# Optimization experiments

Measured on AMD Instinct MI355X. Metric: run time of the kernel, lower is better.

The kernel has to match this reference:

```python
import jax, jax.numpy as jnp
import numpy as np

TEXT_DIM = 1024
FEAT_DIM = 1024
NUM_HEADS = 16
HEAD_DIM = FEAT_DIM // NUM_HEADS
EPS = 1e-6


def rms_norm(x, w):
    # LlamaRMSNorm: compute in fp32, scale by learned weight
    xf = x.astype(jnp.float32)
    var = jnp.mean(xf * xf, axis=-1, keepdims=True)
    return (xf * jax.lax.rsqrt(var + EPS)).astype(x.dtype) * w


def setup_inputs() -> dict:
    key = jax.random.key(0)
    ks = jax.random.split(key, 8)
    def xavier(k, shape, gain=1.0):
        fan_in, fan_out = shape[1], shape[0]
        lim = gain * np.sqrt(6.0 / (fan_in + fan_out))
        return jax.random.uniform(k, shape, jnp.float32, -lim, lim)
    return {
        "text": jax.random.normal(ks[0], (8, 512, TEXT_DIM), jnp.float32),
        "features": jax.random.normal(ks[1], (8, 1024, FEAT_DIM), jnp.float32),
        "W_q": xavier(ks[2], (FEAT_DIM, TEXT_DIM)),
        "b_q": jnp.zeros((FEAT_DIM,), jnp.float32),
        "W_k": xavier(ks[3], (FEAT_DIM, FEAT_DIM)),
        "b_k": jnp.zeros((FEAT_DIM,), jnp.float32),
        "W_o": xavier(ks[4], (FEAT_DIM, FEAT_DIM), gain=0.1),
        "b_o": jnp.zeros((FEAT_DIM,), jnp.float32),
        "g_feat": jnp.ones((FEAT_DIM,), jnp.float32),
        "g_q": jnp.ones((FEAT_DIM,), jnp.float32),
        "g_k": jnp.ones((FEAT_DIM,), jnp.float32),
    }


def reference(text, features, W_q, b_q, W_k, b_k, W_o, b_o, g_feat, g_q, g_k):
    B, T, _ = text.shape
    _, N, _ = features.shape
    feats = rms_norm(features, g_feat)                      # [B,N,Df]
    Q = rms_norm(text @ W_q.T + b_q, g_q)                   # [B,T,Df]
    K = rms_norm(feats @ W_k.T + b_k, g_k)                  # [B,N,Df]
    Qh = Q.reshape(B, T, NUM_HEADS, HEAD_DIM)
    Kh = K.reshape(B, N, NUM_HEADS, HEAD_DIM)
    Vh = feats.reshape(B, N, NUM_HEADS, HEAD_DIM)
    scores = jnp.einsum("bthd,bnhd->bhtn", Qh, Kh) / np.sqrt(HEAD_DIM).astype(np.float32)
    attn = jax.nn.softmax(scores, axis=-1)                  # [B,H,T,N]
    out = jnp.einsum("bhtn,bnhd->bthd", attn, Vh).reshape(B, T, FEAT_DIM)
    return out @ W_o.T + b_o
```

## Files before the change

### kernel.cpp

```cpp
#include <hip/hip_runtime.h>
#include <hip/hip_bf16.h>


typedef unsigned short u16;
typedef __bf16 bf16x8 __attribute__((ext_vector_type(8)));
typedef float f32x4 __attribute__((ext_vector_type(4)));

extern "C" __device__ float __ocml_native_exp2_f32(float);

__device__ inline f32x4 mfma16(bf16x8 a, bf16x8 b, f32x4 c) {
    return __builtin_amdgcn_mfma_f32_16x16x32_bf16(a, b, c, 0, 0, 0);
}

__device__ inline u16 f2bf(float f) {
    union { float f; unsigned u; } v; v.f = f;
    unsigned r = v.u + 0x7fffu + ((v.u >> 16) & 1u);
    return (u16)(r >> 16);
}

__device__ inline unsigned pk_bf16(float a, float b) {
    union { float f; unsigned u; } x, y; x.f = a; y.f = b;
    return __builtin_amdgcn_perm(y.u + 0x8000u, x.u + 0x8000u, 0x07060302u);
}

__device__ inline unsigned cvt_pk(float a, float b) {
    unsigned r;
    asm("v_cvt_pk_bf16_f32 %0, %1, %2" : "=v"(r) : "v"(a), "v"(b));
    return r;
}

__device__ inline void load_lds16(const void* g, void* l) {
    __builtin_amdgcn_global_load_lds(
        (const __attribute__((address_space(1))) void*)g,
        (__attribute__((address_space(3))) void*)l, 16, 0, 0);
}

__global__ __launch_bounds__(256) void cast_rows_kernel(const float* __restrict__ text,
                                                        const float* __restrict__ Wq,
                                                        const float* __restrict__ Wk,
                                                        const float* __restrict__ Wo,
                                                        const float* __restrict__ features,
                                                        const float* __restrict__ g_feat,
                                                        u16* __restrict__ otext, u16* __restrict__ oWq,
                                                        u16* __restrict__ oWk, u16* __restrict__ oWo,
                                                        u16* __restrict__ feats_bf,
                                                        float* __restrict__ qkss) {
    int blk = blockIdx.x, tid = threadIdx.x;
    if (blk < 7168) {
        int i = blk * 256 + tid;
        const float* src; u16* dst; int off;
        if (i < 1048576)      { src = text; dst = otext; off = i; }
        else if (i < 1310720) { src = Wq;   dst = oWq;   off = i - 1048576; }
        else if (i < 1572864) { src = Wk;   dst = oWk;   off = i - 1310720; }
        else                  { src = Wo;   dst = oWo;   off = i - 1572864; }
        float4 v = ((const float4*)src)[off];
        uint2 p; p.x = pk_bf16(v.x, v.y); p.y = pk_bf16(v.z, v.w);
        ((uint2*)dst)[off] = p;
    } else {
        int i2 = (blk - 7168) * 256 + tid;
        if (i2 < 12288) qkss[i2] = 0.0f;
        int row = (blk - 7168) * 4 + (tid >> 6);
        int lane = tid & 63;
        const float4* rp = (const float4*)(features + (size_t)row * 1024) + lane * 4;
        float4 v[4];
        float ss = 0.0f;
        #pragma unroll
        for (int i = 0; i < 4; ++i) {
            v[i] = rp[i];
            ss += v[i].x * v[i].x + v[i].y * v[i].y + v[i].z * v[i].z + v[i].w * v[i].w;
        }
        #pragma unroll
        for (int m = 1; m < 64; m <<= 1) ss += __shfl_xor(ss, m, 64);
        float rs = rsqrtf(ss * (1.0f / 1024.0f) + 1e-6f);
        const float4* gp = (const float4*)(g_feat) + lane * 4;
        union { unsigned u[8]; uint4 q[2]; } ob;
        #pragma unroll
        for (int i = 0; i < 4; ++i) {
            float4 gv = gp[i];
            ob.u[i * 2]     = pk_bf16(v[i].x * rs * gv.x, v[i].y * rs * gv.y);
            ob.u[i * 2 + 1] = pk_bf16(v[i].z * rs * gv.z, v[i].w * rs * gv.w);
        }
        uint4* dst = (uint4*)(feats_bf + (size_t)row * 1024 + lane * 16);
        dst[0] = ob.q[0];
        dst[1] = ob.q[1];
    }
}

__global__ __launch_bounds__(256) void normT_kernel(const u16* __restrict__ feats_bf,
                                                    u16* __restrict__ Vt) {
    __shared__ __align__(16) u16 tile[64][72];
    int tid = threadIdx.x, b = blockIdx.z;
    int n0 = blockIdx.x * 64, d0 = blockIdx.y * 64;
    int r = tid >> 2, cs = (tid & 3) * 16;
    int grow = b * 1024 + n0 + r;

    const uint4* src = (const uint4*)(feats_bf + (size_t)grow * 1024 + d0 + cs);
    union { u16 s[16]; uint4 v[2]; } ob;
    ob.v[0] = src[0];
    ob.v[1] = src[1];
    #pragma unroll
    for (int i = 0; i < 16; ++i) tile[r][cs + i] = ob.s[i];
    __syncthreads();
    union { u16 s[8]; uint4 v; } t0, t1;
    #pragma unroll
    for (int i = 0; i < 8; ++i) { t0.s[i] = tile[cs + i][r]; t1.s[i] = tile[cs + 8 + i][r]; }
    u16* tdst = Vt + ((size_t)(b * 1024 + d0 + r)) * 1024 + n0 + cs;
    *(uint4*)tdst = t0.v;
    *(uint4*)(tdst + 8) = t1.v;
}

template <bool BF16OUT, bool NORM>
__device__ __forceinline__ void gemm64_bk64(const u16* __restrict__ A, const u16* __restrict__ B,
                                            const float* __restrict__ bias,
                                            const float* __restrict__ gvec,
                                            float* __restrict__ ssout,
                                            void* __restrict__ Cout,
                                            int m_blk, int n_blk, int K, int N,
                                            u16* As, u16* Bs) {
    int tid = threadIdx.x, wave = tid >> 6, lane = tid & 63;
    int quad = lane >> 4, l15 = lane & 15;
    int wm = wave & 1, wn = wave >> 1;
    int srl = lane >> 3, scl = lane & 7;
    const int swz = (scl ^ srl) * 8;

    f32x4 acc[4][2] = {};

    auto stage = [&](int buf, int k0) {
        u16* Ad = As + buf * (128 * 64);
        u16* Bd = Bs + buf * (64 * 64);
        #pragma unroll
        for (int is = 0; is < 4; ++is) {
            int row = is * 32 + wave * 8 + srl;
            load_lds16(A + (size_t)(m_blk + row) * K + k0 + swz,
                       Ad + (is * 32 + wave * 8) * 64);
        }
        #pragma unroll
        for (int is = 0; is < 2; ++is) {
            int row = is * 32 + wave * 8 + srl;
            load_lds16(B + (size_t)(n_blk + row) * K + k0 + swz,
                       Bd + (is * 32 + wave * 8) * 64);
        }
    };

    stage(0, 0);
    __syncthreads();
    int cur = 0;

    for (int k0 = 0; k0 < K; k0 += 64) {
        if (k0 + 64 < K) stage(cur ^ 1, k0 + 64);

        const u16* Ar = As + cur * (128 * 64);
        const u16* Br = Bs + cur * (64 * 64);
        #pragma unroll
        for (int kh = 0; kh < 2; ++kh) {
            bf16x8 af[4], bfr[2];
            int co = ((kh * 4 + quad) ^ (l15 & 7)) * 8;
            #pragma unroll
            for (int t = 0; t < 4; ++t)
                af[t] = *(const bf16x8*)&Ar[(wm * 64 + t * 16 + l15) * 64 + co];
            #pragma unroll
            for (int t = 0; t < 2; ++t)
                bfr[t] = *(const bf16x8*)&Br[(wn * 32 + t * 16 + l15) * 64 + co];
            #pragma unroll
            for (int mt = 0; mt < 4; ++mt)
                #pragma unroll
                for (int nt = 0; nt < 2; ++nt)
                    acc[mt][nt] = mfma16(af[mt], bfr[nt], acc[mt][nt]);
        }
        __syncthreads();
        cur ^= 1;
    }

    float bv[2], gv[2];
    #pragma unroll
    for (int nt = 0; nt < 2; ++nt) {
        int col = n_blk + wn * 32 + nt * 16 + l15;
        bv[nt] = bias[col];
        if (NORM) gv[nt] = gvec[col];
    }
    #pragma unroll
    for (int mt = 0; mt < 4; ++mt) {
        int row0 = m_blk + wm * 64 + mt * 16 + quad * 4;
        #pragma unroll
        for (int nt = 0; nt < 2; ++nt)
            #pragma unroll
            for (int r = 0; r < 4; ++r)
                acc[mt][nt][r] += bv[nt];
        if (NORM) {
            f32x4 ss4 = {0.0f, 0.0f, 0.0f, 0.0f};
            #pragma unroll
            for (int nt = 0; nt < 2; ++nt)
                #pragma unroll
                for (int r = 0; r < 4; ++r)
                    ss4[r] += acc[mt][nt][r] * acc[mt][nt][r];
            #pragma unroll
            for (int m = 1; m < 16; m <<= 1)
                #pragma unroll
                for (int r = 0; r < 4; ++r)
                    ss4[r] += __shfl_xor(ss4[r], m, 64);
            if (l15 == 0) {
                #pragma unroll
                for (int r = 0; r < 4; ++r)
                    atomicAdd(&ssout[row0 + r], ss4[r]);
            }
        }
        #pragma unroll
        for (int nt = 0; nt < 2; ++nt) {
            int col = n_blk + wn * 32 + nt * 16 + l15;
            #pragma unroll
            for (int r = 0; r < 4; ++r) {
                float val = NORM ? acc[mt][nt][r] * gv[nt] : acc[mt][nt][r];
                if (BF16OUT) ((u16*)Cout)[(size_t)(row0 + r) * N + col] = f2bf(val);
                else       ((float*)Cout)[(size_t)(row0 + r) * N + col] = val;
            }
        }
    }
}

__global__ __launch_bounds__(256) void gemm_qk_kernel(const u16* __restrict__ text_bf,
                                                      const u16* __restrict__ Wq,
                                                      const u16* __restrict__ feats_bf,
                                                      const u16* __restrict__ Wk,
                                                      const float* __restrict__ b_q,
                                                      const float* __restrict__ b_k,
                                                      const float* __restrict__ g_q,
                                                      const float* __restrict__ g_k,
                                                      float* __restrict__ qkss,
                                                      u16* __restrict__ QK) {
    __shared__ __align__(16) u16 As[2 * 128 * 64];
    __shared__ __align__(16) u16 Bs[2 * 64 * 64];
    int id = blockIdx.x;
    if (id < 512) {
        gemm64_bk64<true, true>(text_bf, Wq, b_q, g_q, qkss, QK,
                                (id & 31) * 128, (id >> 5) * 64, 1024, 1024, As, Bs);
    } else {
        id -= 512;
        gemm64_bk64<true, true>(feats_bf, Wk, b_k, g_k, qkss + 4096, QK + 4096 * 1024,
                                (id & 63) * 128, (id >> 6) * 64, 1024, 1024, As, Bs);
    }
}

__global__ __launch_bounds__(256) void gemm_o_kernel(const u16* __restrict__ A,
                                                     const u16* __restrict__ B,
                                                     const float* __restrict__ bias,
                                                     float* __restrict__ C) {
    __shared__ __align__(16) u16 As[2 * 128 * 64];
    __shared__ __align__(16) u16 Bs[2 * 64 * 64];
    int id = blockIdx.x;
    gemm64_bk64<false, false>(A, B, bias, nullptr, nullptr, C,
                              (id & 31) * 128, (id >> 5) * 64, 1024, 1024, As, Bs);
}

__global__ __launch_bounds__(256, 4) void attn_kernel(const u16* __restrict__ Q,
                                                      const u16* __restrict__ K,
                                                      const u16* __restrict__ Vt,
                                                      const float* __restrict__ qkss,
                                                      u16* __restrict__ Out) {
    const float QSCALE = 0.18033688011112042f;
    int bh = blockIdx.x, qt = blockIdx.y;
    int b = bh >> 4, h = bh & 15;
    int tid = threadIdx.x, wave = tid >> 6, lane = tid & 63;
    int quad = lane >> 4, l15 = lane & 15;
    int wq = wave & 1, wn = wave >> 1;

    __shared__ __align__(16) u16 Ks[2][64 * 64];
    __shared__ __align__(16) u16 Vs[2][64 * 64];
    __shared__ __align__(16) u16 Plds[4][2 * 16 * 32];
    u16* Pw = &Plds[wave][0];
    const int pfs = (l15 >> 1) & 3;

    bf16x8 qf[2][2];
    float rsq[2];
    #pragma unroll
    for (int mt = 0; mt < 2; ++mt) {
        int qrow = b * 512 + qt * 64 + wq * 32 + mt * 16 + l15;
        const size_t qoff = (size_t)qrow * 1024 + h * 64 + quad * 8;
        qf[mt][0] = *(const bf16x8*)(Q + qoff);
        qf[mt][1] = *(const bf16x8*)(Q + qoff + 32);
        rsq[mt] = rsqrtf(qkss[qrow] * (1.0f / 1024.0f) + 1e-6f) * QSCALE;
    }
    const float* ssk = qkss + 4096 + b * 1024;

    int srl = lane >> 3, scl = lane & 7;
    const u16* Kbase = K + ((size_t)(b * 1024)) * 1024 + h * 64;
    const u16* Vbase = Vt + ((size_t)(b * 1024 + h * 64)) * 1024;

    __bf16 onev = (__bf16)1.0f;
    bf16x8 ones = {onev, onev, onev, onev, onev, onev, onev, onev};

    f32x4 o[2][4] = {};
    f32x4 lac[2] = {{0.0f, 0.0f, 0.0f, 0.0f}, {0.0f, 0.0f, 0.0f, 0.0f}};

    auto stage = [&](int buf, int n0) {
        #pragma unroll
        for (int j = 0; j < 2; ++j) {
            int row = wave * 16 + j * 8 + srl;
            load_lds16(Kbase + (size_t)(n0 + row) * 1024 + (scl ^ srl) * 8,
                       &Ks[buf][(wave * 16 + j * 8) * 64]);
            load_lds16(Vbase + (size_t)row * 1024 + n0 + (scl ^ srl) * 8,
                       &Vs[buf][(wave * 16 + j * 8) * 64]);
        }
    };

    stage(0, 0);
    __syncthreads();
    int cur = 0;

    for (int n0 = 0; n0 < 1024; n0 += 64) {
        if (n0 < 960) stage(cur ^ 1, n0 + 64);

        f32x4 s[2][2];
        __builtin_amdgcn_s_setprio(1);
        #pragma unroll
        for (int nt = 0; nt < 2; ++nt) {
            int R = wn * 32 + nt * 16 + l15;
            int c1 = (quad ^ (l15 & 7)) * 8;
            bf16x8 kf0 = *(const bf16x8*)&Ks[cur][R * 64 + c1];
            bf16x8 kf1 = *(const bf16x8*)&Ks[cur][R * 64 + (c1 ^ 32)];
            #pragma unroll
            for (int mt = 0; mt < 2; ++mt) {
                f32x4 z = {0.0f, 0.0f, 0.0f, 0.0f};
                s[mt][nt] = mfma16(kf0, qf[mt][0], z);
                s[mt][nt] = mfma16(kf1, qf[mt][1], s[mt][nt]);
            }
        }
        __builtin_amdgcn_s_setprio(0);

        #pragma unroll
        for (int nt = 0; nt < 2; ++nt) {
            int nb = n0 + wn * 32 + nt * 16 + quad * 4;
            f32x4 kss = *(const f32x4*)&ssk[nb];
            f32x4 rsn;
            #pragma unroll
            for (int r = 0; r < 4; ++r)
                rsn[r] = rsqrtf(kss[r] * (1.0f / 1024.0f) + 1e-6f);
            #pragma unroll
            for (int mt = 0; mt < 2; ++mt) {
                float e[4];
                #pragma unroll
                for (int r = 0; r < 4; ++r)
                    e[r] = __ocml_native_exp2_f32(fmaf(s[mt][nt][r], rsn[r] * rsq[mt], -16.0f));
                uint2 pk;
                pk.x = cvt_pk(e[0], e[1]);
                pk.y = cvt_pk(e[2], e[3]);
                *(uint2*)&Pw[mt * 512 + l15 * 32 + (((nt * 4 + quad) ^ (pfs << 1)) << 2)] = pk;
            }
        }

        bf16x8 pf[2], vf[4];
        #pragma unroll
        for (int mt = 0; mt < 2; ++mt)
            pf[mt] = *(const bf16x8*)&Pw[mt * 512 + l15 * 32 + ((quad ^ pfs) << 3)];
        #pragma unroll
        for (int dt = 0; dt < 4; ++dt) {
            int ch = ((wn * 4 + quad) ^ (l15 & 7)) * 8;
            vf[dt] = *(const bf16x8*)&Vs[cur][(dt * 16 + l15) * 64 + ch];
        }
        __builtin_amdgcn_s_setprio(1);
        #pragma unroll
        for (int mt = 0; mt < 2; ++mt) {
            lac[mt] = mfma16(ones, pf[mt], lac[mt]);
            #pragma unroll
            for (int dt = 0; dt < 4; ++dt)
                o[mt][dt] = mfma16(vf[dt], pf[mt], o[mt][dt]);
        }
        __builtin_amdgcn_s_setprio(0);

        __syncthreads();
        cur ^= 1;
    }

    float* Ored = (float*)&Ks[0][0];
    float* Lred = (float*)&Vs[0][0];
    if (wn == 1) {
        #pragma unroll
        for (int mt = 0; mt < 2; ++mt) {
            #pragma unroll
            for (int dt = 0; dt < 4; ++dt) {
                int c = mt * 4 + dt;
                *(f32x4*)&Ored[wq * 2048 + lane * 32 + ((c ^ (lane & 7)) << 2)] = o[mt][dt];
            }
            Lred[wq * 128 + lane * 2 + mt] = lac[mt][0];
        }
    }
    __syncthreads();
    if (wn == 0) {
        #pragma unroll
        for (int mt = 0; mt < 2; ++mt) {
            float il = 1.0f / (lac[mt][0] + Lred[wq * 128 + lane * 2 + mt]);
            size_t obase =
                ((size_t)(b * 512 + qt * 64 + wq * 32 + mt * 16 + l15)) * 1024 + h * 64 + quad * 4;
            #pragma unroll
            for (int dt = 0; dt < 4; ++dt) {
                int c = mt * 4 + dt;
                f32x4 oo = o[mt][dt] + *(const f32x4*)&Ored[wq * 2048 + lane * 32 + ((c ^ (lane & 7)) << 2)];
                uint2 pk;
                pk.x = cvt_pk(oo[0] * il, oo[1] * il);
                pk.y = cvt_pk(oo[2] * il, oo[3] * il);
                *(uint2*)(Out + obase + dt * 16) = pk;
            }
        }
    }
}

extern "C" void kernel_launch(void* const* d_in, const int* in_sizes, int n_in,
                              void* d_out, int out_size, void* d_ws, size_t ws_size,
                              hipStream_t stream) {
    const float* text     = (const float*)d_in[0];
    const float* features = (const float*)d_in[1];
    const float* W_q      = (const float*)d_in[2];
    const float* b_q      = (const float*)d_in[3];
    const float* W_k      = (const float*)d_in[4];
    const float* b_k      = (const float*)d_in[5];
    const float* W_o      = (const float*)d_in[6];
    const float* b_o      = (const float*)d_in[7];
    const float* g_feat   = (const float*)d_in[8];
    const float* g_q      = (const float*)d_in[9];
    const float* g_k      = (const float*)d_in[10];

    char* ws = (char*)d_ws;
    u16*   text_bf  = (u16*)(ws + 0);
    u16*   Wq_bf    = (u16*)(ws + 8388608);
    u16*   Wk_bf    = (u16*)(ws + 10485760);
    u16*   Wo_bf    = (u16*)(ws + 12582912);
    u16*   feats_bf = (u16*)(ws + 14680064);
    u16*   Vt       = (u16*)(ws + 31457280);
    u16*   QKbuf    = (u16*)(ws + 48234496);
    u16*   attn_bf  = (u16*)(ws + 73400320);
    float* qkss     = (float*)(ws + 81821696);

    cast_rows_kernel<<<9216, 256, 0, stream>>>(text, W_q, W_k, W_o, features, g_feat,
                                               text_bf, Wq_bf, Wk_bf, Wo_bf,
                                               feats_bf, qkss);
    normT_kernel<<<dim3(16, 16, 8), 256, 0, stream>>>(feats_bf, Vt);
    gemm_qk_kernel<<<1536, 256, 0, stream>>>(text_bf, Wq_bf, feats_bf, Wk_bf,
                                             b_q, b_k, g_q, g_k, qkss, QKbuf);
    attn_kernel<<<dim3(128, 8), 256, 0, stream>>>(QKbuf, QKbuf + 4096 * 1024, Vt, qkss, attn_bf);
    gemm_o_kernel<<<512, 256, 0, stream>>>(attn_bf, Wo_bf, b_o, (float*)d_out);
}
```

Before: 219.8 us.

## Keep P in registers via zero-padded MFMA operands, split keys across all four waves

Each wave now covers 16 key columns for all 64 queries, instead of a 2x2 query/key wave split. The score MFMA output layout is reused directly as the B operand of the PV MFMA, with the upper half zero-padded, which removes the per-iteration P round trip through LDS. V fragments are loaded as half-width reads that match this layout. The final reduction now combines four waves' partials through LDS. The trade-off is half-wasted MFMA K-depth in the PV product, more accumulator registers, and dropping the occupancy hint in launch bounds.

New measurement: 227.5 us. +3.5%, slower.

```diff
diff --git a/kernel.cpp b/kernel.cpp
--- a/kernel.cpp
+++ b/kernel.cpp
@@ -5,6 +5,7 @@
 typedef unsigned short u16;
 typedef __bf16 bf16x8 __attribute__((ext_vector_type(8)));
 typedef float f32x4 __attribute__((ext_vector_type(4)));
+typedef unsigned u32x2 __attribute__((ext_vector_type(2)));
 
 extern "C" __device__ float __ocml_native_exp2_f32(float);
 
@@ -27,6 +28,12 @@
     unsigned r;
     asm("v_cvt_pk_bf16_f32 %0, %1, %2" : "=v"(r) : "v"(a), "v"(b));
     return r;
+}
+
+__device__ inline bf16x8 pad4(unsigned lo, unsigned hi) {
+    union { unsigned u[4]; bf16x8 v; } t;
+    t.u[0] = lo; t.u[1] = hi; t.u[2] = 0u; t.u[3] = 0u;
+    return t.v;
 }
 
 __device__ inline void load_lds16(const void* g, void* l) {
@@ -251,29 +258,26 @@
                               (id & 31) * 128, (id >> 5) * 64, 1024, 1024, As, Bs);
 }
 
-__global__ __launch_bounds__(256, 4) void attn_kernel(const u16* __restrict__ Q,
-                                                      const u16* __restrict__ K,
-                                                      const u16* __restrict__ Vt,
-                                                      const float* __restrict__ qkss,
-                                                      u16* __restrict__ Out) {
+__global__ __launch_bounds__(256) void attn_kernel(const u16* __restrict__ Q,
+                                                   const u16* __restrict__ K,
+                                                   const u16* __restrict__ Vt,
+                                                   const float* __restrict__ qkss,
+                                                   u16* __restrict__ Out) {
     const float QSCALE = 0.18033688011112042f;
     int bh = blockIdx.x, qt = blockIdx.y;
     int b = bh >> 4, h = bh & 15;
     int tid = threadIdx.x, wave = tid >> 6, lane = tid & 63;
     int quad = lane >> 4, l15 = lane & 15;
-    int wq = wave & 1, wn = wave >> 1;
-
-    __shared__ __align__(16) u16 Ks[2][64 * 64];
-    __shared__ __align__(16) u16 Vs[2][64 * 64];
-    __shared__ __align__(16) u16 Plds[4][2 * 16 * 32];
-    u16* Pw = &Plds[wave][0];
-    const int pfs = (l15 >> 1) & 3;
-
-    bf16x8 qf[2][2];
-    float rsq[2];
+
+    __shared__ __align__(16) char smem[35840];
+    u16* Ks = (u16*)smem;
+    u16* Vs = Ks + 2 * 64 * 64;
+
+    bf16x8 qf[4][2];
+    float rsq[4];
     #pragma unroll
-    for (int mt = 0; mt < 2; ++mt) {
-        int qrow = b * 512 + qt * 64 + wq * 32 + mt * 16 + l15;
+    for (int mt = 0; mt < 4; ++mt) {
+        int qrow = b * 512 + qt * 64 + mt * 16 + l15;
         const size_t qoff = (size_t)qrow * 1024 + h * 64 + quad * 8;
         qf[mt][0] = *(const bf16x8*)(Q + qoff);
         qf[mt][1] = *(const bf16x8*)(Q + qoff + 32);
@@ -285,20 +289,19 @@
     const u16* Kbase = K + ((size_t)(b * 1024)) * 1024 + h * 64;
     const u16* Vbase = Vt + ((size_t)(b * 1024 + h * 64)) * 1024;
 
-    __bf16 onev = (__bf16)1.0f;
-    bf16x8 ones = {onev, onev, onev, onev, onev, onev, onev, onev};
-
-    f32x4 o[2][4] = {};
-    f32x4 lac[2] = {{0.0f, 0.0f, 0.0f, 0.0f}, {0.0f, 0.0f, 0.0f, 0.0f}};
+    const bf16x8 ones4 = pad4(0x3F803F80u, 0x3F803F80u);
+
+    f32x4 o[4][4] = {};
+    f32x4 lac[4] = {};
 
     auto stage = [&](int buf, int n0) {
         #pragma unroll
         for (int j = 0; j < 2; ++j) {
             int row = wave * 16 + j * 8 + srl;
             load_lds16(Kbase + (size_t)(n0 + row) * 1024 + (scl ^ srl) * 8,
-                       &Ks[buf][(wave * 16 + j * 8) * 64]);
+                       Ks + buf * 4096 + (wave * 16 + j * 8) * 64);
             load_lds16(Vbase + (size_t)row * 1024 + n0 + (scl ^ srl) * 8,
-                       &Vs[buf][(wave * 16 + j * 8) * 64]);
+                       Vs + buf * 4096 + (wave * 16 + j * 8) * 64);
         }
     };
 
@@ -306,60 +309,55 @@
     __syncthreads();
     int cur = 0;
 
+    const int vsw = (quad & 1) * 4;
+
     for (int n0 = 0; n0 < 1024; n0 += 64) {
         if (n0 < 960) stage(cur ^ 1, n0 + 64);
 
-        f32x4 s[2][2];
+        f32x4 s[4];
         __builtin_amdgcn_s_setprio(1);
-        #pragma unroll
-        for (int nt = 0; nt < 2; ++nt) {
-            int R = wn * 32 + nt * 16 + l15;
+        {
+            int R = wave * 16 + l15;
             int c1 = (quad ^ (l15 & 7)) * 8;
-            bf16x8 kf0 = *(const bf16x8*)&Ks[cur][R * 64 + c1];
-            bf16x8 kf1 = *(const bf16x8*)&Ks[cur][R * 64 + (c1 ^ 32)];
-            #pragma unroll
-            for (int mt = 0; mt < 2; ++mt) {
+            bf16x8 kf0 = *(const bf16x8*)&Ks[cur * 4096 + R * 64 + c1];
+            bf16x8 kf1 = *(const bf16x8*)&Ks[cur * 4096 + R * 64 + (c1 ^ 32)];
+            #pragma unroll
+            for (int mt = 0; mt < 4; ++mt) {
                 f32x4 z = {0.0f, 0.0f, 0.0f, 0.0f};
-                s[mt][nt] = mfma16(kf0, qf[mt][0], z);
-                s[mt][nt] = mfma16(kf1, qf[mt][1], s[mt][nt]);
+                s[mt] = mfma16(kf0, qf[mt][0], z);
+                s[mt] = mfma16(kf1, qf[mt][1], s[mt]);
             }
         }
         __builtin_amdgcn_s_setprio(0);
 
-        #pragma unroll
-        for (int nt = 0; nt < 2; ++nt) {
-            int nb = n0 + wn * 32 + nt * 16 + quad * 4;
-            f32x4 kss = *(const f32x4*)&ssk[nb];
-            f32x4 rsn;
+        f32x4 kss = *(const f32x4*)&ssk[n0 + wave * 16 + quad * 4];
+        f32x4 rsn;
+        #pragma unroll
+        for (int r = 0; r < 4; ++r)
+            rsn[r] = rsqrtf(kss[r] * (1.0f / 1024.0f) + 1e-6f);
+        bf16x8 pf[4];
+        #pragma unroll
+        for (int mt = 0; mt < 4; ++mt) {
+            float e[4];
             #pragma unroll
             for (int r = 0; r < 4; ++r)
-                rsn[r] = rsqrtf(kss[r] * (1.0f / 1024.0f) + 1e-6f);
-            #pragma unroll
-            for (int mt = 0; mt < 2; ++mt) {
-                float e[4];
-                #pragma unroll
-                for (int r = 0; r < 4; ++r)
-                    e[r] = __ocml_native_exp2_f32(fmaf(s[mt][nt][r], rsn[r] * rsq[mt], -16.0f));
-                uint2 pk;
-                pk.x = cvt_pk(e[0], e[1]);
-                pk.y = cvt_pk(e[2], e[3]);
-                *(uint2*)&Pw[mt * 512 + l15 * 32 + (((nt * 4 + quad) ^ (pfs << 1)) << 2)] = pk;
-            }
-        }
-
-        bf16x8 pf[2], vf[4];
-        #pragma unroll
-        for (int mt = 0; mt < 2; ++mt)
-            pf[mt] = *(const bf16x8*)&Pw[mt * 512 + l15 * 32 + ((quad ^ pfs) << 3)];
+                e[r] = __ocml_native_exp2_f32(fmaf(s[mt][r], rsn[r] * rsq[mt], -16.0f));
+            pf[mt] = pad4(cvt_pk(e[0], e[1]), cvt_pk(e[2], e[3]));
+        }
+
+        bf16x8 vf[4];
         #pragma unroll
         for (int dt = 0; dt < 4; ++dt) {
-            int ch = ((wn * 4 + quad) ^ (l15 & 7)) * 8;
-            vf[dt] = *(const bf16x8*)&Vs[cur][(dt * 16 + l15) * 64 + ch];
-        }
+            int rowv = dt * 16 + l15;
+            int ch = (wave * 2 + (quad >> 1)) ^ (l15 & 7);
+            u32x2 vraw = *(const u32x2*)&Vs[cur * 4096 + rowv * 64 + ch * 8 + vsw];
+            vf[dt] = pad4(vraw[0], vraw[1]);
+        }
+
         __builtin_amdgcn_s_setprio(1);
         #pragma unroll
-        for (int mt = 0; mt < 2; ++mt) {
-            lac[mt] = mfma16(ones, pf[mt], lac[mt]);
+        for (int mt = 0; mt < 4; ++mt) {
+            lac[mt] = mfma16(ones4, pf[mt], lac[mt]);
             #pragma unroll
             for (int dt = 0; dt < 4; ++dt)
                 o[mt][dt] = mfma16(vf[dt], pf[mt], o[mt][dt]);
@@ -370,36 +368,54 @@
         cur ^= 1;
     }
 
-    float* Ored = (float*)&Ks[0][0];
-    float* Lred = (float*)&Vs[0][0];
-    if (wn == 1) {
-        #pragma unroll
-        for (int mt = 0; mt < 2; ++mt) {
-            #pragma unroll
-            for (int dt = 0; dt < 4; ++dt) {
-                int c = mt * 4 + dt;
-                *(f32x4*)&Ored[wq * 2048 + lane * 32 + ((c ^ (lane & 7)) << 2)] = o[mt][dt];
-            }
-            Lred[wq * 128 + lane * 2 + mt] = lac[mt][0];
+    float* R0   = (float*)smem;
+    float* R1   = R0 + 64 * 68;
+    float* lacb = R1 + 64 * 68;
+
+    if (wave >= 2) {
+        float* R = (wave == 2) ? R0 : R1;
+        #pragma unroll
+        for (int mt = 0; mt < 4; ++mt) {
+            #pragma unroll
+            for (int dt = 0; dt < 4; ++dt)
+                #pragma unroll
+                for (int r = 0; r < 4; ++r)
+                    R[(dt * 16 + quad * 4 + r) * 68 + mt * 16 + l15] = o[mt][dt][r];
+            if (quad == 0) lacb[wave * 64 + mt * 16 + l15] = lac[mt][0];
         }
     }
     __syncthreads();
-    if (wn == 0) {
-        #pragma unroll
-        for (int mt = 0; mt < 2; ++mt) {
-            float il = 1.0f / (lac[mt][0] + Lred[wq * 128 + lane * 2 + mt]);
-            size_t obase =
-                ((size_t)(b * 512 + qt * 64 + wq * 32 + mt * 16 + l15)) * 1024 + h * 64 + quad * 4;
-            #pragma unroll
-            for (int dt = 0; dt < 4; ++dt) {
-                int c = mt * 4 + dt;
-                f32x4 oo = o[mt][dt] + *(const f32x4*)&Ored[wq * 2048 + lane * 32 + ((c ^ (lane & 7)) << 2)];
-                uint2 pk;
-                pk.x = cvt_pk(oo[0] * il, oo[1] * il);
-                pk.y = cvt_pk(oo[2] * il, oo[3] * il);
-                *(uint2*)(Out + obase + dt * 16) = pk;
-            }
-        }
+    if (wave < 2) {
+        float* R = (wave == 0) ? R0 : R1;
+        #pragma unroll
+        for (int mt = 0; mt < 4; ++mt) {
+            #pragma unroll
+            for (int dt = 0; dt < 4; ++dt)
+                #pragma unroll
+                for (int r = 0; r < 4; ++r) {
+                    int ix = (dt * 16 + quad * 4 + r) * 68 + mt * 16 + l15;
+                    R[ix] += o[mt][dt][r];
+                }
+            if (quad == 0)
+                lacb[wave * 64 + mt * 16 + l15] =
+                    lac[mt][0] + lacb[(wave + 2) * 64 + mt * 16 + l15];
+        }
+    }
+    __syncthreads();
+    {
+        int q = wave * 16 + l15;
+        float il = 1.0f / (lacb[q] + lacb[64 + q]);
+        union { unsigned u[8]; uint4 v[2]; } pk;
+        #pragma unroll
+        for (int j = 0; j < 8; ++j) {
+            int d0 = quad * 16 + 2 * j;
+            float v0 = (R0[d0 * 68 + q] + R1[d0 * 68 + q]) * il;
+            float v1 = (R0[(d0 + 1) * 68 + q] + R1[(d0 + 1) * 68 + q]) * il;
+            pk.u[j] = cvt_pk(v0, v1);
+        }
+        size_t orow = ((size_t)(b * 512 + qt * 64 + q)) * 1024 + h * 64 + quad * 16;
+        *(uint4*)(Out + orow) = pk.v[0];
+        *(uint4*)(Out + orow + 8) = pk.v[1];
     }
 }
 
```
